# Performance work log

Hardware: AMD Instinct MI355X
Metric: run time of the kernel (lower is better)

The kernel has to match this reference:

```python
import jax, jax.numpy as jnp
import numpy as np

N = 100000      # nodes
E = 1200000     # directed edges (before self loops)
IN = 128        # in_channels
POS = 16        # pos_dim
H = 4           # heads
OUT = 16        # out_channels per head
NEG_SLOPE = 0.2
DIV_W = 0.1


def setup_inputs() -> dict:
    key = jax.random.key(0)
    k0, k1, k2, k3, k4 = jax.random.split(key, 5)
    x = jax.random.normal(k0, (N, IN), jnp.float32)
    edge_index = jax.random.randint(k1, (2, E), 0, N, dtype=jnp.int64)
    W = jax.random.normal(k2, (IN - POS, H * OUT), jnp.float32) * (1.0 / np.sqrt(IN - POS).astype(np.float32))
    att = jax.random.normal(k3, (1, H, 2 * OUT), jnp.float32) * 0.1
    pos_att = jax.random.normal(k4, (1, H, 2 * POS), jnp.float32) * 0.1
    bias = jnp.zeros((H * OUT,), jnp.float32)
    return {"x": x, "edge_index": edge_index, "W": W, "att": att, "pos_att": pos_att, "bias": bias}


def _segment_softmax(scores, seg, n):
    # numerically stable softmax over segments defined by seg (per source node, as in the torch code)
    m = jax.ops.segment_max(scores, seg, num_segments=n)           # [n, H]
    e = jnp.exp(scores - m[seg])                                   # [E', H]
    s = jax.ops.segment_sum(e, seg, num_segments=n)                # [n, H]
    return e / (s[seg] + 1e-10)


def _diversity_loss(alpha):
    # pairwise correlations between L2-normalized per-head attention vectors,
    # diagonal left at zero, mean over full HxH matrix (matches torch loop)
    norm = jnp.maximum(jnp.linalg.norm(alpha, axis=0, keepdims=True), 1e-12)
    a = alpha / norm                                               # [E', H]
    gram = a.T @ a                                                 # [H, H]
    gram = gram * (1.0 - jnp.eye(H, dtype=gram.dtype))
    return jnp.mean(gram) * DIV_W


def reference(x, edge_index, W, att, pos_att, bias):
    n = x.shape[0]
    loops = jnp.arange(n, dtype=edge_index.dtype)
    row = jnp.concatenate([edge_index[0], loops])                  # [E'] = E + N
    col = jnp.concatenate([edge_index[1], loops])

    content = (x[:, :-POS] @ W).reshape(n, H, OUT)                 # [n, H, OUT]
    pos = x[:, -POS:]                                              # [n, POS]

    # concat([c_i, c_j]) . att == c_i . att[:OUT] + c_j . att[OUT:]  (compute per-node, gather per-edge)
    s_ci = jnp.einsum('nhd,hd->nh', content, att[0, :, :OUT])
    s_cj = jnp.einsum('nhd,hd->nh', content, att[0, :, OUT:])
    s_pi = pos @ pos_att[0, :, :POS].T                             # [n, H]
    s_pj = pos @ pos_att[0, :, POS:].T

    alpha = (s_ci + s_pi)[row] + (s_cj + s_pj)[col]                # [E', H]
    alpha = jax.nn.leaky_relu(alpha, NEG_SLOPE)
    alpha = _segment_softmax(alpha, row, n)

    diversity_loss = _diversity_loss(alpha)

    # message: x_j * alpha (x_j = content[source] = content[row]); aggregate: scatter-add at target (col)
    msgs = content[row] * alpha[:, :, None]                        # [E', H, OUT]
    out = jax.ops.segment_sum(msgs, col, num_segments=n)           # [n, H, OUT]
    out = out.reshape(n, H * OUT) + bias
    return (out, diversity_loss)
```

## Files before the change

### kernel.cpp

```cpp
#include <hip/hip_runtime.h>
#include <hip/hip_fp16.h>

#define NN   100000
#define NE   1200000
#define MT   (NE + NN)
#define HH   4
#define HD   64
#define NEG_SLOPE 0.2f
#define NGB  25000
#define SBLK 1024
#define EPB  1270
#define NCB  782
#define NBKT 782
#define BCAP 2048

static __device__ __forceinline__ unsigned short f2bf(float f) {
    unsigned int b = __float_as_uint(f);
    b += 0x7FFFu + ((b >> 16) & 1u);
    return (unsigned short)(b >> 16);
}
static __device__ __forceinline__ float h_lo(unsigned w) {
    return __half2float(__ushort_as_half((unsigned short)(w & 0xffff)));
}
static __device__ __forceinline__ float h_hi(unsigned w) {
    return __half2float(__ushort_as_half((unsigned short)(w >> 16)));
}
static __device__ __forceinline__ unsigned pack_h2(float a, float b) {
    return (unsigned)__half_as_ushort(__float2half(a)) |
           ((unsigned)__half_as_ushort(__float2half(b)) << 16);
}

__global__ __launch_bounds__(256) void k_fused(
    const float* __restrict__ x, const float* __restrict__ W,
    const float* __restrict__ att, const float* __restrict__ pos_att,
    const int* __restrict__ ei,
    unsigned* __restrict__ regionD, unsigned* __restrict__ regionR,
    unsigned short* __restrict__ offD16, unsigned short* __restrict__ offR16,
    unsigned short* __restrict__ contentb, __half* __restrict__ nd,
    __half* __restrict__ sjh)
{
    __shared__ __align__(16) char smem[45056];
    const int t = threadIdx.x;

    if (blockIdx.x < SBLK) {
        unsigned* scan = (unsigned*)smem;
        unsigned* curs = (unsigned*)(smem + 8192);
        unsigned* stD  = (unsigned*)(smem + 14448);
        unsigned* stR  = (unsigned*)(smem + 19568);
        const int p  = blockIdx.x;
        const int e0 = p * EPB;
        const int e1 = min(e0 + EPB, MT);
        for (int i = t; i < 2048; i += 256) scan[i] = 0;
        __syncthreads();
        int er[5], ec[5];
        #pragma unroll
        for (int k = 0; k < 5; ++k) {
            const int e = e0 + t + k * 256;
            if (e < e1) {
                int r, c;
                if (e < NE) {
                    r = __builtin_nontemporal_load(ei + e);
                    c = __builtin_nontemporal_load(ei + NE + e);
                } else { r = e - NE; c = r; }
                er[k] = r; ec[k] = c;
                atomicAdd(&scan[c >> 7], 1u);
                atomicAdd(&scan[1024 + (r >> 7)], 1u);
            } else er[k] = -1;
        }
        __syncthreads();
        for (int s = 1; s < 2048; s <<= 1) {
            unsigned v[8];
            #pragma unroll
            for (int k = 0; k < 8; ++k) {
                const int i = t + k * 256;
                v[k] = (i >= s) ? scan[i - s] : 0u;
            }
            __syncthreads();
            #pragma unroll
            for (int k = 0; k < 8; ++k) scan[t + k * 256] += v[k];
            __syncthreads();
        }
        const unsigned totD  = scan[1023];
        const unsigned base_ = scan[1023];
        const unsigned totR  = scan[2047] - base_;
        for (int i = t; i < NBKT; i += 256) {
            const unsigned dstart = (i == 0) ? 0u : scan[i - 1];
            const unsigned rstart = ((i == 0) ? base_ : scan[1024 + i - 1]) - base_;
            curs[i]         = dstart;
            curs[NBKT + i]  = rstart;
            offD16[(size_t)p * (NBKT + 1) + i] = (unsigned short)dstart;
            offR16[(size_t)p * (NBKT + 1) + i] = (unsigned short)rstart;
        }
        if (t == 0) {
            offD16[(size_t)p * (NBKT + 1) + NBKT] = (unsigned short)totD;
            offR16[(size_t)p * (NBKT + 1) + NBKT] = (unsigned short)totR;
        }
        __syncthreads();
        #pragma unroll
        for (int k = 0; k < 5; ++k) {
            if (er[k] >= 0) {
                const unsigned pd = atomicAdd(&curs[ec[k] >> 7], 1u);
                stD[pd] = (unsigned)er[k] | ((unsigned)(ec[k] & 127) << 17);
                const unsigned pr = atomicAdd(&curs[NBKT + (er[k] >> 7)], 1u);
                stR[pr] = (unsigned)ec[k] | ((unsigned)(er[k] & 127) << 17);
            }
        }
        __syncthreads();
        for (unsigned i = t; i < totD; i += 256)
            regionD[(size_t)p * EPB + i] = stD[i];
        for (unsigned i = t; i < totR; i += 256)
            regionR[(size_t)p * EPB + i] = stR[i];
        return;
    }

    float* Wl  = (float*)smem;
    float* xsT = (float*)(smem + 28672);
    for (int i = t; i < 112 * 64; i += 256) Wl[i] = W[i];

    const int gb  = blockIdx.x - SBLK;
    const int n0  = gb * 128;
    const int oc  = (t & 7) * 8;
    const int h   = oc >> 4;
    const int ng4 = (t >> 3) * 4;

    float acc[4][8];
    #pragma unroll
    for (int j = 0; j < 4; ++j)
        #pragma unroll
        for (int o = 0; o < 8; ++o) acc[j][o] = 0.f;

    for (int ph = 0; ph < 4; ++ph) {
        __syncthreads();
        for (int idx = t; idx < 128 * 32; idx += 256) {
            const int nl = idx >> 5;
            const int kk = idx & 31;
            const int gn = n0 + nl;
            const float v = (gn < NN) ? x[(size_t)gn * 128 + ph * 32 + kk] : 0.f;
            xsT[kk * 128 + (nl ^ (kk << 2))] = v;
        }
        __syncthreads();
        const int klim = (ph == 3) ? 16 : 32;
        #pragma unroll 4
        for (int kk = 0; kk < klim; ++kk) {
            const int sw = kk << 2;
            const float4 xv = *(const float4*)&xsT[kk * 128 + (ng4 ^ sw)];
            const int kg = ph * 32 + kk;
            const float4 w0 = *(const float4*)&Wl[kg * 64 + oc];
            const float4 w1 = *(const float4*)&Wl[kg * 64 + oc + 4];
            const float xa[4] = { xv.x, xv.y, xv.z, xv.w };
            #pragma unroll
            for (int j = 0; j < 4; ++j) {
                acc[j][0] = fmaf(xa[j], w0.x, acc[j][0]);
                acc[j][1] = fmaf(xa[j], w0.y, acc[j][1]);
                acc[j][2] = fmaf(xa[j], w0.z, acc[j][2]);
                acc[j][3] = fmaf(xa[j], w0.w, acc[j][3]);
                acc[j][4] = fmaf(xa[j], w1.x, acc[j][4]);
                acc[j][5] = fmaf(xa[j], w1.y, acc[j][5]);
                acc[j][6] = fmaf(xa[j], w1.z, acc[j][6]);
                acc[j][7] = fmaf(xa[j], w1.w, acc[j][7]);
            }
        }
    }

    const int dbase = oc & 15;
    float ati[8], atj[8], pti[8], ptj[8];
    #pragma unroll
    for (int j = 0; j < 8; ++j) {
        ati[j] = att[h * 32 + dbase + j];
        atj[j] = att[h * 32 + 16 + dbase + j];
        pti[j] = pos_att[h * 32 + dbase + j];
        ptj[j] = pos_att[h * 32 + 16 + dbase + j];
    }
    #pragma unroll
    for (int j = 0; j < 4; ++j) {
        const int gn = n0 + ng4 + j;
        float s1 = 0.f, s2 = 0.f;
        #pragma unroll
        for (int o = 0; o < 8; ++o) {
            s1 = fmaf(acc[j][o], ati[o], s1);
            s2 = fmaf(acc[j][o], atj[o], s2);
        }
        #pragma unroll
        for (int pp = 0; pp < 8; ++pp) {
            const int r3 = 16 + dbase + pp;
            const float pv = xsT[r3 * 128 + ((ng4 + j) ^ (r3 << 2))];
            s1 = fmaf(pv, pti[pp], s1);
            s2 = fmaf(pv, ptj[pp], s2);
        }
        s1 += __shfl_xor(s1, 1);
        s2 += __shfl_xor(s2, 1);
        if (gn < NN) {
            if ((t & 1) == 0) nd[(size_t)gn * 8 + h]  = __float2half(s1);
            else              sjh[(size_t)gn * 4 + h] = __float2half(s2);
            uint4 pk;
            pk.x = (unsigned)f2bf(acc[j][0]) | ((unsigned)f2bf(acc[j][1]) << 16);
            pk.y = (unsigned)f2bf(acc[j][2]) | ((unsigned)f2bf(acc[j][3]) << 16);
            pk.z = (unsigned)f2bf(acc[j][4]) | ((unsigned)f2bf(acc[j][5]) << 16);
            pk.w = (unsigned)f2bf(acc[j][6]) | ((unsigned)f2bf(acc[j][7]) << 16);
            *(uint4*)&contentb[(size_t)gn * 64 + oc] = pk;
        }
    }
}

__global__ __launch_bounds__(256) void k_pass2(
    const unsigned* __restrict__ regionD, const unsigned* __restrict__ regionR,
    const unsigned short* __restrict__ offD16, const unsigned short* __restrict__ offR16,
    __half* __restrict__ nd, const __half* __restrict__ sjh,
    unsigned* __restrict__ sortedC, int* __restrict__ nodeoff,
    int* __restrict__ nodedeg, int* __restrict__ btot)
{
    __shared__ __align__(16) char smem[17920];
    const int t = threadIdx.x;

    if (blockIdx.x < NBKT) {
        const int g = blockIdx.x;
        unsigned* cnt   = (unsigned*)smem;
        unsigned* curs  = (unsigned*)(smem + 512);
        unsigned* rawc  = (unsigned*)(smem + 1024);
        unsigned* raw   = (unsigned*)(smem + 1536);
        unsigned* srt   = (unsigned*)(smem + 1536 + BCAP * 4);
        if (t < 128) cnt[t] = 0;
        if (t == 0) rawc[0] = 0;
        __syncthreads();
        for (int pb = t; pb < SBLK; pb += 256) {
            const int o0 = offD16[(size_t)pb * (NBKT + 1) + g];
            const int o1 = offD16[(size_t)pb * (NBKT + 1) + g + 1];
            const int s  = o1 - o0;
            if (s > 0) {
                const unsigned base = atomicAdd(rawc, (unsigned)s);
                if (base + s <= BCAP) {
                    for (int i = 0; i < s; ++i) {
                        const unsigned rec = regionD[(size_t)pb * EPB + o0 + i];
                        raw[base + i] = rec;
                        atomicAdd(&cnt[rec >> 17], 1u);
                    }
                }
            }
        }
        __syncthreads();
        const unsigned total = min(rawc[0], (unsigned)BCAP);
        if (t < 128) curs[t] = cnt[t];
        __syncthreads();
        for (int s = 1; s < 128; s <<= 1) {
            unsigned v = 0;
            if (t < 128 && t >= s) v = curs[t - s];
            __syncthreads();
            if (t < 128) curs[t] += v;
            __syncthreads();
        }
        if (t < 128) {
            const unsigned start = curs[t] - cnt[t];
            const int node = g * 128 + t;
            if (node < NN) {
                nodeoff[node] = g * BCAP + (int)start;
                nodedeg[node] = (int)cnt[t];
            }
            curs[t] = start;
        }
        if (t == 0) btot[g] = (int)total;
        __syncthreads();
        for (unsigned i = t; i < total; i += 256) {
            const unsigned rec = raw[i];
            const unsigned pos = atomicAdd(&curs[rec >> 17], 1u);
            srt[pos] = rec;
        }
        __syncthreads();
        for (unsigned i = t; i < total; i += 256)
            sortedC[(size_t)g * BCAP + i] = srt[i];
        return;
    }

    const int g = blockIdx.x - NBKT;
    float* den = (float*)smem;
    float* siL = (float*)(smem + 2048);
    for (int i = t; i < 512; i += 256) den[i] = 0.f;
    if (t < 128) {
        const int node = g * 128 + t;
        if (node < NN) {
            const uint2 sv = *(const uint2*)(nd + (size_t)node * 8);
            siL[t * 4 + 0] = h_lo(sv.x); siL[t * 4 + 1] = h_hi(sv.x);
            siL[t * 4 + 2] = h_lo(sv.y); siL[t * 4 + 3] = h_hi(sv.y);
        } else {
            siL[t * 4 + 0] = 0.f; siL[t * 4 + 1] = 0.f;
            siL[t * 4 + 2] = 0.f; siL[t * 4 + 3] = 0.f;
        }
    }
    __syncthreads();
    for (int pb = t; pb < SBLK; pb += 256) {
        const int o0 = offR16[(size_t)pb * (NBKT + 1) + g];
        const int o1 = offR16[(size_t)pb * (NBKT + 1) + g + 1];
        for (int i = o0; i < o1; ++i) {
            const unsigned rec = regionR[(size_t)pb * EPB + i];
            const int c    = (int)(rec & 0x1FFFFu);
            const int lrow = (int)(rec >> 17);
            const uint2 jv = *(const uint2*)(sjh + (size_t)c * 4);
            float v0 = siL[lrow * 4 + 0] + h_lo(jv.x);
            float v1 = siL[lrow * 4 + 1] + h_hi(jv.x);
            float v2 = siL[lrow * 4 + 2] + h_lo(jv.y);
            float v3 = siL[lrow * 4 + 3] + h_hi(jv.y);
            v0 = v0 > 0.f ? v0 : NEG_SLOPE * v0;
            v1 = v1 > 0.f ? v1 : NEG_SLOPE * v1;
            v2 = v2 > 0.f ? v2 : NEG_SLOPE * v2;
            v3 = v3 > 0.f ? v3 : NEG_SLOPE * v3;
            atomicAdd(&den[lrow * 4 + 0], __expf(v0));
            atomicAdd(&den[lrow * 4 + 1], __expf(v1));
            atomicAdd(&den[lrow * 4 + 2], __expf(v2));
            atomicAdd(&den[lrow * 4 + 3], __expf(v3));
        }
    }
    __syncthreads();
    if (t < 128) {
        const int node = g * 128 + t;
        if (node < NN) {
            uint2 dv;
            dv.x = pack_h2(den[t * 4 + 0], den[t * 4 + 1]);
            dv.y = pack_h2(den[t * 4 + 2], den[t * 4 + 3]);
            *(uint2*)(nd + (size_t)node * 8 + 4) = dv;
        }
    }
}

__global__ __launch_bounds__(256) void k_alpha(
    const unsigned* __restrict__ sortedC, const int* __restrict__ btot,
    const __half* __restrict__ nd, const __half* __restrict__ sjh,
    uint2* __restrict__ sortedA, float* __restrict__ gpart)
{
    __shared__ uint2 sjL[128];
    __shared__ float red[4][10];
    const int t = threadIdx.x;
    const int g = blockIdx.x >> 1;
    const int q = blockIdx.x & 1;
    if (t < 128) {
        const int node = g * 128 + t;
        uint2 z; z.x = 0; z.y = 0;
        sjL[t] = (node < NN) ? *(const uint2*)(sjh + (size_t)node * 4) : z;
    }
    __syncthreads();
    const int total = btot[g];
    float a0=0,a1=0,a2=0,a3=0,a4=0,a5=0,a6=0,a7=0,a8=0,a9=0;
    for (int i = q * 256 + t; i < total; i += 512) {
        const unsigned rec = sortedC[(size_t)g * BCAP + i];
        const int r    = (int)(rec & 0x1FFFFu);
        const int lrow = (int)(rec >> 17);
        const uint4 nr = *(const uint4*)(nd + (size_t)r * 8);
        const uint2 jv = sjL[lrow];
        float v0 = h_lo(nr.x) + h_lo(jv.x);
        float v1 = h_hi(nr.x) + h_hi(jv.x);
        float v2 = h_lo(nr.y) + h_lo(jv.y);
        float v3 = h_hi(nr.y) + h_hi(jv.y);
        v0 = v0 > 0.f ? v0 : NEG_SLOPE * v0;
        v1 = v1 > 0.f ? v1 : NEG_SLOPE * v1;
        v2 = v2 > 0.f ? v2 : NEG_SLOPE * v2;
        v3 = v3 > 0.f ? v3 : NEG_SLOPE * v3;
        const float al0 = __expf(v0) / (h_lo(nr.z) + 1e-10f);
        const float al1 = __expf(v1) / (h_hi(nr.z) + 1e-10f);
        const float al2 = __expf(v2) / (h_lo(nr.w) + 1e-10f);
        const float al3 = __expf(v3) / (h_hi(nr.w) + 1e-10f);
        uint2 aw;
        aw.x = pack_h2(al0, al1);
        aw.y = pack_h2(al2, al3);
        sortedA[(size_t)g * BCAP + i] = aw;
        a0=fmaf(al0,al0,a0); a1=fmaf(al0,al1,a1); a2=fmaf(al0,al2,a2); a3=fmaf(al0,al3,a3);
        a4=fmaf(al1,al1,a4); a5=fmaf(al1,al2,a5); a6=fmaf(al1,al3,a6);
        a7=fmaf(al2,al2,a7); a8=fmaf(al2,al3,a8); a9=fmaf(al3,al3,a9);
    }
    #pragma unroll
    for (int m = 32; m >= 1; m >>= 1) {
        a0 += __shfl_xor(a0, m); a1 += __shfl_xor(a1, m);
        a2 += __shfl_xor(a2, m); a3 += __shfl_xor(a3, m);
        a4 += __shfl_xor(a4, m); a5 += __shfl_xor(a5, m);
        a6 += __shfl_xor(a6, m); a7 += __shfl_xor(a7, m);
        a8 += __shfl_xor(a8, m); a9 += __shfl_xor(a9, m);
    }
    const int lane = t & 63, wid = t >> 6;
    if (lane == 0) {
        red[wid][0]=a0; red[wid][1]=a1; red[wid][2]=a2; red[wid][3]=a3; red[wid][4]=a4;
        red[wid][5]=a5; red[wid][6]=a6; red[wid][7]=a7; red[wid][8]=a8; red[wid][9]=a9;
    }
    __syncthreads();
    if (t < 10)
        gpart[(size_t)blockIdx.x * 10 + t] =
            red[0][t] + red[1][t] + red[2][t] + red[3][t];
}

__global__ __launch_bounds__(256) void k_gather(
    const int* __restrict__ nodeoff, const int* __restrict__ nodedeg,
    const unsigned* __restrict__ sortedC, const uint2* __restrict__ sortedA,
    const unsigned short* __restrict__ contentb, const float* __restrict__ bias,
    float* __restrict__ out)
{
    const int lane = threadIdx.x & 63;
    const int wid  = threadIdx.x >> 6;
    const int n    = blockIdx.x * 4 + wid;
    const int h    = lane >> 4;
    const int start = __builtin_amdgcn_readfirstlane(nodeoff[n]);
    const int cd    = __builtin_amdgcn_readfirstlane(min(nodedeg[n], 64));
    float acc = 0.f;

    int j = 0;
    for (; j + 7 < cd; j += 8) {
        unsigned rec[8];
        uint2 aw[8];
        float cv[8];
        #pragma unroll
        for (int k = 0; k < 8; ++k) rec[k] = sortedC[(size_t)start + j + k];
        #pragma unroll
        for (int k = 0; k < 8; ++k) aw[k] = sortedA[(size_t)start + j + k];
        #pragma unroll
        for (int k = 0; k < 8; ++k)
            cv[k] = __uint_as_float(
                (unsigned)contentb[(size_t)(rec[k] & 0x1FFFFu) * 64 + lane] << 16);
        #pragma unroll
        for (int k = 0; k < 8; ++k) {
            const unsigned w = (h & 2) ? aw[k].y : aw[k].x;
            const float al = (h & 1) ? h_hi(w) : h_lo(w);
            acc = fmaf(cv[k], al, acc);
        }
    }
    for (; j < cd; ++j) {
        const unsigned rec = sortedC[(size_t)start + j];
        const uint2 aw = sortedA[(size_t)start + j];
        const unsigned w = (h & 2) ? aw.y : aw.x;
        const float al = (h & 1) ? h_hi(w) : h_lo(w);
        const float cvv = __uint_as_float(
            (unsigned)contentb[(size_t)(rec & 0x1FFFFu) * 64 + lane] << 16);
        acc = fmaf(cvv, al, acc);
    }
    out[(size_t)n * 64 + lane] = acc + bias[lane];
}

__global__ __launch_bounds__(256) void k_gred(
    const float* __restrict__ gpart, double* __restrict__ pairs)
{
    const int row = blockIdx.x * 256 + threadIdx.x;
    float v[10];
    #pragma unroll
    for (int i = 0; i < 10; ++i)
        v[i] = (row < 2 * NBKT) ? gpart[(size_t)row * 10 + i] : 0.f;
    #pragma unroll
    for (int m = 32; m >= 1; m >>= 1)
        #pragma unroll
        for (int i = 0; i < 10; ++i) v[i] += __shfl_xor(v[i], m);
    __shared__ float red[4][10];
    const int lane = threadIdx.x & 63, wid = threadIdx.x >> 6;
    if (lane == 0)
        #pragma unroll
        for (int i = 0; i < 10; ++i) red[wid][i] = v[i];
    __syncthreads();
    if (threadIdx.x < 10) {
        const double s = (double)red[0][threadIdx.x] + red[1][threadIdx.x]
                       + red[2][threadIdx.x] + red[3][threadIdx.x];
        atomicAdd(pairs + threadIdx.x, s);
    }
}

__global__ void k_loss(const double* __restrict__ ps, float* __restrict__ out)
{
    if (threadIdx.x == 0 && blockIdx.x == 0) {
        const double s00=ps[0], s01=ps[1], s02=ps[2], s03=ps[3], s11=ps[4];
        const double s12=ps[5], s13=ps[6], s22=ps[7], s23=ps[8], s33=ps[9];
        const double n0 = fmax(sqrt(s00), 1e-12);
        const double n1 = fmax(sqrt(s11), 1e-12);
        const double n2 = fmax(sqrt(s22), 1e-12);
        const double n3 = fmax(sqrt(s33), 1e-12);
        double loss = 2.0 * ( s01/(n0*n1) + s02/(n0*n2) + s03/(n0*n3)
                            + s12/(n1*n2) + s13/(n1*n3) + s23/(n2*n3) );
        loss = loss / 16.0 * 0.1;
        out[NN * HD] = (float)loss;
    }
}

extern "C" void kernel_launch(void* const* d_in, const int* in_sizes, int n_in,
                              void* d_out, int out_size, void* d_ws, size_t ws_size,
                              hipStream_t stream)
{
    const float* x       = (const float*)d_in[0];
    const int*   ei      = (const int*)d_in[1];
    const float* W       = (const float*)d_in[2];
    const float* att     = (const float*)d_in[3];
    const float* pos_att = (const float*)d_in[4];
    const float* bias    = (const float*)d_in[5];
    float* out = (float*)d_out;

    char* p = (char*)d_ws;
    double* pairs = (double*)p;              p += 128;
    __half* nd    = (__half*)p;              p += (size_t)NN * 8 * 2;
    __half* sjh   = (__half*)p;              p += (size_t)NN * 4 * 2;
    float*  gpart = (float*)p;               p += (size_t)2 * NBKT * 10 * 4 + 64;
    unsigned short* contentb = (unsigned short*)p; p += (size_t)NN * 64 * 2;
    unsigned* regionD = (unsigned*)p;        p += (size_t)SBLK * EPB * 4;
    unsigned* regionR = (unsigned*)p;        p += (size_t)SBLK * EPB * 4;
    unsigned short* offD16 = (unsigned short*)p; p += (size_t)SBLK * (NBKT+1) * 2;
    unsigned short* offR16 = (unsigned short*)p; p += (size_t)SBLK * (NBKT+1) * 2;
    unsigned* sortedC = (unsigned*)p;        p += (size_t)NBKT * BCAP * 4;
    uint2*   sortedA = (uint2*)p;            p += (size_t)NBKT * BCAP * 8;
    int* nodeoff = (int*)p;                  p += (size_t)NN * 4;
    int* nodedeg = (int*)p;                  p += (size_t)NN * 4;
    int* btot    = (int*)p;                  p += (size_t)NBKT * 4 + 64;

    (void)hipMemsetAsync(pairs, 0, 128, stream);

    k_fused <<<SBLK + NCB, 256, 0, stream>>>(x, W, att, pos_att, ei,
                                             regionD, regionR, offD16, offR16,
                                             contentb, nd, sjh);
    k_pass2 <<<2 * NBKT, 256, 0, stream>>>(regionD, regionR, offD16, offR16,
                                           nd, sjh, sortedC, nodeoff, nodedeg, btot);
    k_alpha <<<2 * NBKT, 256, 0, stream>>>(sortedC, btot, nd, sjh, sortedA, gpart);
    k_gather<<<NGB, 256, 0, stream>>>(nodeoff, nodedeg, sortedC, sortedA,
                                      contentb, bias, out);
    k_gred  <<<(2 * NBKT + 255) / 256, 256, 0, stream>>>(gpart, pairs);
    k_loss  <<<1, 64, 0, stream>>>(pairs, out);
}
```

Before: 278.8 us.

## Use wave-shuffle prefix scan and process two nodes per wave in gather

The block-wide Hillis-Steele scan over 2048 shared-memory bucket counters, which used eleven barrier-separated passes, becomes a per-thread serial scan of 8 entries plus a wave-level shuffle scan and a cross-wave combine. The gather kernel now has each wavefront accumulate two destination nodes at once in chunks of 4 edges, so loads for both nodes are in flight together and more memory-level parallelism is exposed. In exchange the gather carries extra branching and register pressure, and load imbalance when the two nodes have different degrees. There is also leftover dead code (the unused `a` predicate).

```diff
diff --git a/kernel.cpp b/kernel.cpp
--- a/kernel.cpp
+++ b/kernel.cpp
@@ -7,7 +7,6 @@
 #define HH   4
 #define HD   64
 #define NEG_SLOPE 0.2f
-#define NGB  25000
 #define SBLK 1024
 #define EPB  1270
 #define NCB  782
@@ -47,6 +46,7 @@
         unsigned* curs = (unsigned*)(smem + 8192);
         unsigned* stD  = (unsigned*)(smem + 14448);
         unsigned* stR  = (unsigned*)(smem + 19568);
+        unsigned* wtot = (unsigned*)(smem + 24688);
         const int p  = blockIdx.x;
         const int e0 = p * EPB;
         const int e1 = min(e0 + EPB, MT);
@@ -68,18 +68,26 @@
             } else er[k] = -1;
         }
         __syncthreads();
-        for (int s = 1; s < 2048; s <<= 1) {
-            unsigned v[8];
-            #pragma unroll
-            for (int k = 0; k < 8; ++k) {
-                const int i = t + k * 256;
-                v[k] = (i >= s) ? scan[i - s] : 0u;
-            }
-            __syncthreads();
-            #pragma unroll
-            for (int k = 0; k < 8; ++k) scan[t + k * 256] += v[k];
-            __syncthreads();
-        }
+        const int lane = t & 63, wv = t >> 6;
+        unsigned lpre[8];
+        unsigned run = 0;
+        #pragma unroll
+        for (int k = 0; k < 8; ++k) { run += scan[t * 8 + k]; lpre[k] = run; }
+        unsigned sc = run;
+        #pragma unroll
+        for (int d = 1; d < 64; d <<= 1) {
+            const unsigned u = __shfl_up(sc, d);
+            if (lane >= d) sc += u;
+        }
+        if (lane == 63) wtot[wv] = sc;
+        __syncthreads();
+        unsigned wbase = 0;
+        for (int k = 0; k < wv; ++k) wbase += wtot[k];
+        const unsigned tbase = wbase + sc - run;
+        #pragma unroll
+        for (int k = 0; k < 8; ++k) scan[t * 8 + k] = tbase + lpre[k];
+        __syncthreads();
+
         const unsigned totD  = scan[1023];
         const unsigned base_ = scan[1023];
         const unsigned totR  = scan[2047] - base_;
@@ -390,43 +398,86 @@
     float* __restrict__ out)
 {
     const int lane = threadIdx.x & 63;
-    const int wid  = threadIdx.x >> 6;
-    const int n    = blockIdx.x * 4 + wid;
+    const int wv   = threadIdx.x >> 6;
+    const int nb   = blockIdx.x * 8 + wv * 2;
     const int h    = lane >> 4;
-    const int start = __builtin_amdgcn_readfirstlane(nodeoff[n]);
-    const int cd    = __builtin_amdgcn_readfirstlane(min(nodedeg[n], 64));
-    float acc = 0.f;
-
-    int j = 0;
-    for (; j + 7 < cd; j += 8) {
-        unsigned rec[8];
-        uint2 aw[8];
-        float cv[8];
-        #pragma unroll
-        for (int k = 0; k < 8; ++k) rec[k] = sortedC[(size_t)start + j + k];
-        #pragma unroll
-        for (int k = 0; k < 8; ++k) aw[k] = sortedA[(size_t)start + j + k];
-        #pragma unroll
-        for (int k = 0; k < 8; ++k)
-            cv[k] = __uint_as_float(
-                (unsigned)contentb[(size_t)(rec[k] & 0x1FFFFu) * 64 + lane] << 16);
-        #pragma unroll
-        for (int k = 0; k < 8; ++k) {
-            const unsigned w = (h & 2) ? aw[k].y : aw[k].x;
-            const float al = (h & 1) ? h_hi(w) : h_lo(w);
-            acc = fmaf(cv[k], al, acc);
-        }
-    }
-    for (; j < cd; ++j) {
-        const unsigned rec = sortedC[(size_t)start + j];
-        const uint2 aw = sortedA[(size_t)start + j];
+    const int s0 = __builtin_amdgcn_readfirstlane(nodeoff[nb]);
+    const int c0 = __builtin_amdgcn_readfirstlane(min(nodedeg[nb], 64));
+    const int s1 = __builtin_amdgcn_readfirstlane(nodeoff[nb + 1]);
+    const int c1 = __builtin_amdgcn_readfirstlane(min(nodedeg[nb + 1], 64));
+    float acc0 = 0.f, acc1 = 0.f;
+    const int cmax = max(c0, c1);
+
+    for (int jm = 0; jm + 3 < cmax; jm += 4) {
+        const bool a = (jm + 3 < c0) || (jm + 4 == c0) || (jm + 3 == c0 - 1);
+        const bool ga = (jm + 4 <= c0);
+        const bool gb = (jm + 4 <= c1);
+        (void)a;
+        unsigned recA[4], recB[4];
+        uint2 awA[4], awB[4];
+        float cvA[4], cvB[4];
+        if (ga) {
+            #pragma unroll
+            for (int k = 0; k < 4; ++k) recA[k] = sortedC[(size_t)s0 + jm + k];
+            #pragma unroll
+            for (int k = 0; k < 4; ++k) awA[k] = sortedA[(size_t)s0 + jm + k];
+        }
+        if (gb) {
+            #pragma unroll
+            for (int k = 0; k < 4; ++k) recB[k] = sortedC[(size_t)s1 + jm + k];
+            #pragma unroll
+            for (int k = 0; k < 4; ++k) awB[k] = sortedA[(size_t)s1 + jm + k];
+        }
+        if (ga) {
+            #pragma unroll
+            for (int k = 0; k < 4; ++k)
+                cvA[k] = __uint_as_float(
+                    (unsigned)contentb[(size_t)(recA[k] & 0x1FFFFu) * 64 + lane] << 16);
+        }
+        if (gb) {
+            #pragma unroll
+            for (int k = 0; k < 4; ++k)
+                cvB[k] = __uint_as_float(
+                    (unsigned)contentb[(size_t)(recB[k] & 0x1FFFFu) * 64 + lane] << 16);
+        }
+        if (ga) {
+            #pragma unroll
+            for (int k = 0; k < 4; ++k) {
+                const unsigned w = (h & 2) ? awA[k].y : awA[k].x;
+                const float al = (h & 1) ? h_hi(w) : h_lo(w);
+                acc0 = fmaf(cvA[k], al, acc0);
+            }
+        }
+        if (gb) {
+            #pragma unroll
+            for (int k = 0; k < 4; ++k) {
+                const unsigned w = (h & 2) ? awB[k].y : awB[k].x;
+                const float al = (h & 1) ? h_hi(w) : h_lo(w);
+                acc1 = fmaf(cvB[k], al, acc1);
+            }
+        }
+    }
+    for (int j = c0 & ~3; j < c0; ++j) {
+        const unsigned rec = sortedC[(size_t)s0 + j];
+        const uint2 aw = sortedA[(size_t)s0 + j];
         const unsigned w = (h & 2) ? aw.y : aw.x;
         const float al = (h & 1) ? h_hi(w) : h_lo(w);
         const float cvv = __uint_as_float(
             (unsigned)contentb[(size_t)(rec & 0x1FFFFu) * 64 + lane] << 16);
-        acc = fmaf(cvv, al, acc);
-    }
-    out[(size_t)n * 64 + lane] = acc + bias[lane];
+        acc0 = fmaf(cvv, al, acc0);
+    }
+    for (int j = c1 & ~3; j < c1; ++j) {
+        const unsigned rec = sortedC[(size_t)s1 + j];
+        const uint2 aw = sortedA[(size_t)s1 + j];
+        const unsigned w = (h & 2) ? aw.y : aw.x;
+        const float al = (h & 1) ? h_hi(w) : h_lo(w);
+        const float cvv = __uint_as_float(
+            (unsigned)contentb[(size_t)(rec & 0x1FFFFu) * 64 + lane] << 16);
+        acc1 = fmaf(cvv, al, acc1);
+    }
+    const float bv = bias[lane];
+    out[(size_t)nb * 64 + lane]       = acc0 + bv;
+    out[(size_t)(nb + 1) * 64 + lane] = acc1 + bv;
 }
 
 __global__ __launch_bounds__(256) void k_gred(
@@ -506,8 +557,8 @@
     k_pass2 <<<2 * NBKT, 256, 0, stream>>>(regionD, regionR, offD16, offR16,
                                            nd, sjh, sortedC, nodeoff, nodedeg, btot);
     k_alpha <<<2 * NBKT, 256, 0, stream>>>(sortedC, btot, nd, sjh, sortedA, gpart);
-    k_gather<<<NGB, 256, 0, stream>>>(nodeoff, nodedeg, sortedC, sortedA,
-                                      contentb, bias, out);
+    k_gather<<<NN / 8, 256, 0, stream>>>(nodeoff, nodedeg, sortedC, sortedA,
+                                         contentb, bias, out);
     k_gred  <<<(2 * NBKT + 255) / 256, 256, 0, stream>>>(gpart, pairs);
     k_loss  <<<1, 64, 0, stream>>>(pairs, out);
 }
```

New measurement: 279.8 us. Within noise of the previous version (+0.4%).
